# Kernel optimization log

Hardware: AMD Instinct MI355X
Metric: run time of the kernel (lower is better)

The kernel has to match this reference:

```python
import jax, jax.numpy as jnp
import numpy as np

BN_EPS = 1e-5

def conv1x1(w, b, x):
    # w: [O, C], b: [O], x: [B, C, H, W] -> [B, O, H, W]
    return jnp.einsum('oc,bchw->bohw', w, x) + b[None, :, None, None]

def setup_inputs() -> dict:
    key = jax.random.key(0)
    ks = jax.random.split(key, 11)
    C, inter = 256, 128
    B, H, W = 16, 64, 32
    s = 0.05
    return {
        'x': jax.random.normal(ks[0], (B, C, H, W), jnp.float32),
        'g_w': jax.random.normal(ks[1], (inter, C), jnp.float32) * s,
        'g_b': jax.random.normal(ks[2], (inter,), jnp.float32) * s,
        'theta_w': jax.random.normal(ks[3], (inter, C), jnp.float32) * s,
        'theta_b': jax.random.normal(ks[4], (inter,), jnp.float32) * s,
        'phi_w': jax.random.normal(ks[5], (inter, C), jnp.float32) * s,
        'phi_b': jax.random.normal(ks[6], (inter,), jnp.float32) * s,
        'W_w': jax.random.normal(ks[7], (C, inter), jnp.float32) * s,
        'W_b': jax.random.normal(ks[8], (C,), jnp.float32) * s,
        'bn_gamma': jax.random.normal(ks[9], (C,), jnp.float32) * s,
        'bn_beta': jax.random.normal(ks[10], (C,), jnp.float32) * s,
    }

def reference(x, g_w, g_b, theta_w, theta_b, phi_w, phi_b, W_w, W_b, bn_gamma, bn_beta):
    B, C, H, W = x.shape
    N = H * W
    inter = g_w.shape[0]
    # 1x1 conv projections, flattened to token sequences
    g_x = conv1x1(g_w, g_b, x).reshape(B, inter, N).transpose(0, 2, 1)        # [B, N, inter]
    theta_x = conv1x1(theta_w, theta_b, x).reshape(B, inter, N).transpose(0, 2, 1)  # [B, N, inter]
    phi_x = conv1x1(phi_w, phi_b, x).reshape(B, inter, N)                      # [B, inter, N]
    # non-local attention: f = theta @ phi / N, then y = f @ g
    f_div_c = jnp.einsum('bnd,bdm->bnm', theta_x, phi_x) / N                   # [B, N, N]
    y = jnp.einsum('bnm,bmd->bnd', f_div_c, g_x)                               # [B, N, inter]
    y = y.transpose(0, 2, 1).reshape(B, inter, H, W)
    # W: 1x1 conv + BatchNorm (training-mode batch statistics)
    z = conv1x1(W_w, W_b, y)                                                   # [B, C, H, W]
    mean = jnp.mean(z, axis=(0, 2, 3), keepdims=True)
    var = jnp.var(z, axis=(0, 2, 3), keepdims=True)
    z_hat = (z - mean) * jax.lax.rsqrt(var + BN_EPS)
    z_bn = z_hat * bn_gamma[None, :, None, None] + bn_beta[None, :, None, None]
    return z_bn + x
```

## Files before the change

kernel.cpp:

```cpp
#include <hip/hip_runtime.h>

typedef unsigned int uint;
typedef unsigned short ushort;
typedef __attribute__((ext_vector_type(8))) short bf16x8;
typedef __attribute__((ext_vector_type(4))) float f32x4;

#define BB 16
#define CC 256
#define II 128
#define NN 2048
#define BN_EPS 1e-5f

#define OFF_GPART 0
#define OFF_SPART 4194304
#define OFF_CP    4210688
#define OFF_STATP 4214784
#define OFF_STAT2 4345856
#define OFF_PT    4346368
#define OFF_R1    4346624
#define OFF_WGB   4346880
#define OFF_ALPHA 4347136
#define OFF_L1    4347152
#define OFF_R2    4351248
#define OFF_FEND  4355344
#define UGRAM 0
#define UE    1048576
#define UFT   1114112
#define UHT   1179648
#define USBF  2228224
#define UXT   3276800
#define UZ    11665408

static __device__ __forceinline__ ushort f2bf(float f) {
    uint u = __float_as_uint(f);
    return (ushort)((u + 0x7FFFu + ((u >> 16) & 1u)) >> 16);
}
static __device__ __forceinline__ uint pack2(float a, float b) {
    return (uint)f2bf(a) | ((uint)f2bf(b) << 16);
}
static __device__ __forceinline__ float bflo(uint w) { return __uint_as_float(w << 16); }
static __device__ __forceinline__ float bfhi(uint w) { return __uint_as_float(w & 0xFFFF0000u); }
static __device__ __forceinline__ float bfu(ushort u) { return __uint_as_float((uint)u << 16); }

#define MICRO_FMA(av, bv) \
    acc[0][0] += av.x * bv.x; acc[0][1] += av.x * bv.y; acc[0][2] += av.x * bv.z; acc[0][3] += av.x * bv.w; \
    acc[1][0] += av.y * bv.x; acc[1][1] += av.y * bv.y; acc[1][2] += av.y * bv.z; acc[1][3] += av.y * bv.w; \
    acc[2][0] += av.z * bv.x; acc[2][1] += av.z * bv.y; acc[2][2] += av.z * bv.z; acc[2][3] += av.z * bv.w; \
    acc[3][0] += av.w * bv.x; acc[3][1] += av.w * bv.y; acc[3][2] += av.w * bv.z; acc[3][3] += av.w * bv.w;

__global__ __launch_bounds__(256) void convert_xt(
    const float* __restrict__ x, ushort* __restrict__ xT)
{
    __shared__ ushort tile[64][72];
    const int t = threadIdx.x;
    const int b = blockIdx.z, c0 = blockIdx.y * 64, n0 = blockIdx.x * 64;
    const int row = t & 63, ch = t >> 6;
    const size_t srcIdx = ((size_t)(b * CC + c0 + row)) * NN + n0 + ch * 16;
    const float4* sp = (const float4*)(x + srcIdx);
    float4 v0 = sp[0], v1 = sp[1], v2 = sp[2], v3 = sp[3];
    uint p[8];
    p[0] = pack2(v0.x, v0.y); p[1] = pack2(v0.z, v0.w);
    p[2] = pack2(v1.x, v1.y); p[3] = pack2(v1.z, v1.w);
    p[4] = pack2(v2.x, v2.y); p[5] = pack2(v2.z, v2.w);
    p[6] = pack2(v3.x, v3.y); p[7] = pack2(v3.z, v3.w);
    uint* tp = (uint*)&tile[row][ch * 16];
    #pragma unroll
    for (int i = 0; i < 8; ++i) tp[i] = p[i];
    __syncthreads();
    const int trow = t & 63, cch = t >> 6;
    uint q[8];
    #pragma unroll
    for (int i = 0; i < 8; ++i) {
        ushort lo = tile[cch * 16 + 2*i][trow];
        ushort hi = tile[cch * 16 + 2*i + 1][trow];
        q[i] = (uint)lo | ((uint)hi << 16);
    }
    uint4* op = (uint4*)(xT + ((size_t)(b * NN + n0 + trow)) * CC + c0 + cch * 16);
    op[0] = make_uint4(q[0], q[1], q[2], q[3]);
    op[1] = make_uint4(q[4], q[5], q[6], q[7]);
}

__global__ __launch_bounds__(256) void gram_mfma(
    const float* __restrict__ x, float* __restrict__ gpart, float* __restrict__ sPart)
{
    __shared__ ushort As[128][40];
    __shared__ ushort Bs[128][40];
    const int t = threadIdx.x;
    const int jt = blockIdx.x, it = blockIdx.y;
    const int b = blockIdx.z >> 2, kc = blockIdx.z & 3;
    const int iBase = it * 128, jBase = jt * 128;
    const int arow = t >> 1, ah = t & 1;
    const float* aSrc = x + ((size_t)(b * CC + iBase + arow)) * NN + kc * 512 + ah * 16;
    const float* bSrc = x + ((size_t)(b * CC + jBase + arow)) * NN + kc * 512 + ah * 16;
    const int lane = t & 63, wid = t >> 6;
    const int mb = (wid >> 1) * 64, nb = (wid & 1) * 64;
    const int lm = lane & 15, q = lane >> 4;
    f32x4 acc[4][4] = {};
    float ssum = 0.f;

    for (int it16 = 0; it16 < 16; ++it16) {
        const float4* ap = (const float4*)(aSrc + it16 * 32);
        float4 a0 = ap[0], a1 = ap[1], a2 = ap[2], a3 = ap[3];
        const float4* bp = (const float4*)(bSrc + it16 * 32);
        float4 b0 = bp[0], b1 = bp[1], b2 = bp[2], b3 = bp[3];
        uint4 pa0 = { pack2(a0.x,a0.y), pack2(a0.z,a0.w), pack2(a1.x,a1.y), pack2(a1.z,a1.w) };
        uint4 pa1 = { pack2(a2.x,a2.y), pack2(a2.z,a2.w), pack2(a3.x,a3.y), pack2(a3.z,a3.w) };
        uint4 pb0 = { pack2(b0.x,b0.y), pack2(b0.z,b0.w), pack2(b1.x,b1.y), pack2(b1.z,b1.w) };
        uint4 pb1 = { pack2(b2.x,b2.y), pack2(b2.z,b2.w), pack2(b3.x,b3.y), pack2(b3.z,b3.w) };
        *(uint4*)&As[arow][ah * 16]     = pa0;
        *(uint4*)&As[arow][ah * 16 + 8] = pa1;
        *(uint4*)&Bs[arow][ah * 16]     = pb0;
        *(uint4*)&Bs[arow][ah * 16 + 8] = pb1;
        if (jt == 0) {
            ssum += a0.x+a0.y+a0.z+a0.w + a1.x+a1.y+a1.z+a1.w
                  + a2.x+a2.y+a2.z+a2.w + a3.x+a3.y+a3.z+a3.w;
        }
        __syncthreads();
        bf16x8 af[4], bf[4];
        #pragma unroll
        for (int mt = 0; mt < 4; ++mt)
            af[mt] = *(const bf16x8*)&As[mb + mt * 16 + lm][q * 8];
        #pragma unroll
        for (int nt = 0; nt < 4; ++nt)
            bf[nt] = *(const bf16x8*)&Bs[nb + nt * 16 + lm][q * 8];
        #pragma unroll
        for (int mt = 0; mt < 4; ++mt)
            #pragma unroll
            for (int nt = 0; nt < 4; ++nt)
                acc[mt][nt] = __builtin_amdgcn_mfma_f32_16x16x32_bf16(af[mt], bf[nt], acc[mt][nt], 0, 0, 0);
        __syncthreads();
    }
    float* gp = gpart + ((size_t)kc * BB + b) * CC * CC;
    #pragma unroll
    for (int mt = 0; mt < 4; ++mt)
        #pragma unroll
        for (int nt = 0; nt < 4; ++nt)
            #pragma unroll
            for (int r = 0; r < 4; ++r) {
                const int gi = iBase + mb + mt * 16 + q * 4 + r;
                const int gj = jBase + nb + nt * 16 + lm;
                gp[(size_t)gi * CC + gj] = acc[mt][nt][r];
            }
    if (jt == 0) {
        const float so = __shfl_xor(ssum, 1);
        if ((t & 1) == 0)
            sPart[((size_t)kc * BB + b) * CC + iBase + arow] = ssum + so;
    }
}

__global__ __launch_bounds__(256) void gram_reduce(
    const float* __restrict__ gpart, ushort* __restrict__ GramBF)
{
    const int i = blockIdx.x * 256 + threadIdx.x;
    const size_t S = (size_t)BB * CC * CC / 4;
    const float4* p = (const float4*)gpart;
    const float4 a = p[i], b = p[i + S], c = p[i + 2 * S], d = p[i + 3 * S];
    float4 o = { a.x + b.x + c.x + d.x, a.y + b.y + c.y + d.y,
                 a.z + b.z + c.z + d.z, a.w + b.w + c.w + d.w };
    uint2 pk = { pack2(o.x, o.y), pack2(o.z, o.w) };
    ((uint2*)GramBF)[i] = pk;
}

__global__ __launch_bounds__(256) void w1_kernel(
    const float* __restrict__ Ww, const float* __restrict__ Gw,
    const float* __restrict__ Pw, const float* __restrict__ Tw,
    const float* __restrict__ gb, const float* __restrict__ pb, const float* __restrict__ tb,
    ushort* __restrict__ EBF, ushort* __restrict__ FT,
    float* __restrict__ pt, float* __restrict__ r1, float* __restrict__ wgb,
    float* __restrict__ alpha)
{
    const int bz = blockIdx.x;
    const int tid = threadIdx.x;
    if (bz == 32) {
        const int t = tid;
        float ptv = 0.f, r1v = 0.f, wgbv = 0.f;
        for (int d = 0; d < II; ++d) {
            ptv  += Pw[(size_t)d * CC + t] * tb[d];
            r1v  += Tw[(size_t)d * CC + t] * pb[d];
            wgbv += Ww[(size_t)t * II + d] * gb[d];
        }
        pt[t] = ptv; r1[t] = r1v; wgb[t] = wgbv;
        if (t == 0) {
            float al = 0.f;
            for (int d = 0; d < II; ++d) al += pb[d] * tb[d];
            alpha[0] = al;
        }
        return;
    }
    __shared__ float As[32][68];
    __shared__ float Bs[32][68];
    const int a_r = tid >> 2, a_k = (tid & 3) * 8;
    const int b_n = tid & 63, b_k = tid >> 6;
    const int ty = tid >> 4, tx = tid & 15;
    float acc[4][4] = {};
    if (bz < 16) {
        const int cBase = (bz >> 2) * 64, iBase = (bz & 3) * 64;
        const float* ap0 = Ww + (size_t)(cBase + a_r) * II + a_k;
        const float* bp0 = Gw + iBase + b_n;
        for (int k0 = 0; k0 < II; k0 += 32) {
            #pragma unroll
            for (int j = 0; j < 8; ++j) As[a_k + j][a_r] = ap0[k0 + j];
            #pragma unroll
            for (int kk = 0; kk < 8; ++kk) {
                const int k = b_k + kk * 4;
                Bs[k][b_n] = bp0[(size_t)(k0 + k) * CC];
            }
            __syncthreads();
            #pragma unroll
            for (int k = 0; k < 32; ++k) {
                const float4 av = *(const float4*)&As[k][ty * 4];
                const float4 bv = *(const float4*)&Bs[k][tx * 4];
                MICRO_FMA(av, bv)
            }
            __syncthreads();
        }
        #pragma unroll
        for (int ii = 0; ii < 4; ++ii) {
            uint2 o = { pack2(acc[ii][0], acc[ii][1]), pack2(acc[ii][2], acc[ii][3]) };
            *(uint2*)&EBF[(size_t)(cBase + ty * 4 + ii) * CC + iBase + tx * 4] = o;
        }
    } else {
        const int z = bz - 16;
        const int jBase = (z >> 2) * 64, kBase = (z & 3) * 64;
        const float* ap0 = Tw + jBase + b_n;
        const float* bp0 = Pw + kBase + b_n;
        for (int k0 = 0; k0 < II; k0 += 32) {
            #pragma unroll
            for (int kk = 0; kk < 8; ++kk) {
                const int k = b_k + kk * 4;
                As[k][b_n] = ap0[(size_t)(k0 + k) * CC];
                Bs[k][b_n] = bp0[(size_t)(k0 + k) * CC];
            }
            __syncthreads();
            #pragma unroll
            for (int k = 0; k < 32; ++k) {
                const float4 av = *(const float4*)&As[k][ty * 4];
                const float4 bv = *(const float4*)&Bs[k][tx * 4];
                MICRO_FMA(av, bv)
            }
            __syncthreads();
        }
        const float sc = 1.0f / (float)NN;
        #pragma unroll
        for (int ii = 0; ii < 4; ++ii) {
            uint2 o = { pack2(acc[ii][0]*sc, acc[ii][1]*sc), pack2(acc[ii][2]*sc, acc[ii][3]*sc) };
            *(uint2*)&FT[(size_t)(jBase + ty * 4 + ii) * CC + kBase + tx * 4] = o;
        }
    }
}

__global__ __launch_bounds__(256) void u_kernel(
    const float* __restrict__ sPart, const ushort* __restrict__ GramBF,
    const ushort* __restrict__ EBF, const ushort* __restrict__ FT,
    const float* __restrict__ pt, const float* __restrict__ r1,
    const float* __restrict__ wgb, const float* __restrict__ alpha,
    float* __restrict__ cprime, float* __restrict__ L1, float* __restrict__ R2)
{
    __shared__ float sL[256], ptL[256], GptL[256], red[256];
    const int b = blockIdx.x, t = threadIdx.x;
    sL[t] = sPart[(size_t)(0 * BB + b) * CC + t] + sPart[(size_t)(1 * BB + b) * CC + t]
          + sPart[(size_t)(2 * BB + b) * CC + t] + sPart[(size_t)(3 * BB + b) * CC + t];
    ptL[t] = pt[t];
    __syncthreads();
    red[t] = sL[t] * ptL[t];
    __syncthreads();
    for (int s = 128; s > 0; s >>= 1) {
        if (t < s) red[t] += red[t + s];
        __syncthreads();
    }
    const float spt = red[0];
    {
        const uint4* gp = (const uint4*)(GramBF + ((size_t)b * CC + t) * CC);
        float g = 0.f;
        #pragma unroll 4
        for (int kk = 0; kk < 32; ++kk) {
            uint4 v = gp[kk]; const int k = kk * 8;
            g += bflo(v.x)*ptL[k]   + bfhi(v.x)*ptL[k+1] + bflo(v.y)*ptL[k+2] + bfhi(v.y)*ptL[k+3]
               + bflo(v.z)*ptL[k+4] + bfhi(v.z)*ptL[k+5] + bflo(v.w)*ptL[k+6] + bfhi(v.w)*ptL[k+7];
        }
        GptL[t] = g;
    }
    __syncthreads();
    float es = 0.f, eg = 0.f;
    {
        const uint4* ep = (const uint4*)(EBF + (size_t)t * CC);
        #pragma unroll 4
        for (int kk = 0; kk < 32; ++kk) {
            uint4 v = ep[kk]; const int k = kk * 8;
            float e0=bflo(v.x),e1=bfhi(v.x),e2=bflo(v.y),e3=bfhi(v.y);
            float e4=bflo(v.z),e5=bfhi(v.z),e6=bflo(v.w),e7=bfhi(v.w);
            es += e0*sL[k]+e1*sL[k+1]+e2*sL[k+2]+e3*sL[k+3]+e4*sL[k+4]+e5*sL[k+5]+e6*sL[k+6]+e7*sL[k+7];
            eg += e0*GptL[k]+e1*GptL[k+1]+e2*GptL[k+2]+e3*GptL[k+3]+e4*GptL[k+4]+e5*GptL[k+5]+e6*GptL[k+6]+e7*GptL[k+7];
        }
    }
    float r2 = 0.f;
    {
        const uint4* fp = (const uint4*)(FT + (size_t)t * CC);
        #pragma unroll 4
        for (int kk = 0; kk < 32; ++kk) {
            uint4 v = fp[kk]; const int k = kk * 8;
            r2 += bflo(v.x)*sL[k]   + bfhi(v.x)*sL[k+1] + bflo(v.y)*sL[k+2] + bfhi(v.y)*sL[k+3]
                + bflo(v.z)*sL[k+4] + bfhi(v.z)*sL[k+5] + bflo(v.w)*sL[k+6] + bfhi(v.w)*sL[k+7];
        }
    }
    const float al = alpha[0];
    const float wg = wgb[t];
    cprime[b * CC + t] = (eg + al * es + spt * wg) / (float)NN + al * wg;
    L1[b * CC + t] = es / (float)NN;
    R2[b * CC + t] = r2 + r1[t];
}

__global__ __launch_bounds__(256) void h_mfma(
    const ushort* __restrict__ FT, const ushort* __restrict__ GramBF,
    ushort* __restrict__ HT)
{
    __shared__ ushort As[128][40];
    __shared__ ushort Bs[128][40];
    const int t = threadIdx.x;
    const int iBase = blockIdx.x * 128, jBase = blockIdx.y * 128, b = blockIdx.z;
    const int arow = t >> 1, ah = t & 1;
    const ushort* aSrc = FT + (size_t)(jBase + arow) * CC + ah * 16;
    const ushort* bSrc = GramBF + ((size_t)b * CC + iBase + arow) * CC + ah * 16;
    const int lane = t & 63, wid = t >> 6;
    const int mb = (wid >> 1) * 64, nb = (wid & 1) * 64;
    const int lm = lane & 15, q = lane >> 4;
    f32x4 acc[4][4] = {};
    for (int k0 = 0; k0 < CC; k0 += 32) {
        *(uint4*)&As[arow][ah * 16]     = ((const uint4*)(aSrc + k0))[0];
        *(uint4*)&As[arow][ah * 16 + 8] = ((const uint4*)(aSrc + k0))[1];
        *(uint4*)&Bs[arow][ah * 16]     = ((const uint4*)(bSrc + k0))[0];
        *(uint4*)&Bs[arow][ah * 16 + 8] = ((const uint4*)(bSrc + k0))[1];
        __syncthreads();
        bf16x8 af[4], bf[4];
        #pragma unroll
        for (int mt = 0; mt < 4; ++mt)
            af[mt] = *(const bf16x8*)&As[mb + mt * 16 + lm][q * 8];
        #pragma unroll
        for (int nt = 0; nt < 4; ++nt)
            bf[nt] = *(const bf16x8*)&Bs[nb + nt * 16 + lm][q * 8];
        #pragma unroll
        for (int mt = 0; mt < 4; ++mt)
            #pragma unroll
            for (int nt = 0; nt < 4; ++nt)
                acc[mt][nt] = __builtin_amdgcn_mfma_f32_16x16x32_bf16(af[mt], bf[nt], acc[mt][nt], 0, 0, 0);
        __syncthreads();
    }
    ushort* dst = HT + (size_t)b * CC * CC;
    #pragma unroll
    for (int mt = 0; mt < 4; ++mt)
        #pragma unroll
        for (int r = 0; r < 4; ++r) {
            const int j = jBase + mb + mt * 16 + q * 4 + r;
            #pragma unroll
            for (int nt = 0; nt < 4; ++nt) {
                const int i = iBase + nb + nt * 16 + lm;
                dst[(size_t)j * CC + i] = f2bf(acc[mt][nt][r]);
            }
        }
}

__global__ __launch_bounds__(256) void s2_mfma(
    const ushort* __restrict__ EBF, const ushort* __restrict__ HT,
    const float* __restrict__ r1, const float* __restrict__ R2,
    const float* __restrict__ L1, const float* __restrict__ wgb,
    ushort* __restrict__ Sbf)
{
    __shared__ ushort As[128][40];
    __shared__ ushort Bs[128][40];
    const int t = threadIdx.x;
    const int jBase = blockIdx.x * 128, cBase = blockIdx.y * 128, b = blockIdx.z;
    const int arow = t >> 1, ah = t & 1;
    const ushort* aSrc = EBF + (size_t)(cBase + arow) * CC + ah * 16;
    const ushort* bSrc = HT + ((size_t)b * CC + jBase + arow) * CC + ah * 16;
    const int lane = t & 63, wid = t >> 6;
    const int mb = (wid >> 1) * 64, nb = (wid & 1) * 64;
    const int lm = lane & 15, q = lane >> 4;
    f32x4 acc[4][4] = {};
    for (int k0 = 0; k0 < CC; k0 += 32) {
        *(uint4*)&As[arow][ah * 16]     = ((const uint4*)(aSrc + k0))[0];
        *(uint4*)&As[arow][ah * 16 + 8] = ((const uint4*)(aSrc + k0))[1];
        *(uint4*)&Bs[arow][ah * 16]     = ((const uint4*)(bSrc + k0))[0];
        *(uint4*)&Bs[arow][ah * 16 + 8] = ((const uint4*)(bSrc + k0))[1];
        __syncthreads();
        bf16x8 af[4], bf[4];
        #pragma unroll
        for (int mt = 0; mt < 4; ++mt)
            af[mt] = *(const bf16x8*)&As[mb + mt * 16 + lm][q * 8];
        #pragma unroll
        for (int nt = 0; nt < 4; ++nt)
            bf[nt] = *(const bf16x8*)&Bs[nb + nt * 16 + lm][q * 8];
        #pragma unroll
        for (int mt = 0; mt < 4; ++mt)
            #pragma unroll
            for (int nt = 0; nt < 4; ++nt)
                acc[mt][nt] = __builtin_amdgcn_mfma_f32_16x16x32_bf16(af[mt], bf[nt], acc[mt][nt], 0, 0, 0);
        __syncthreads();
    }
    float r1v[4], R2v[4];
    #pragma unroll
    for (int nt = 0; nt < 4; ++nt) {
        const int j = jBase + nb + nt * 16 + lm;
        r1v[nt] = r1[j];
        R2v[nt] = R2[b * CC + j];
    }
    ushort* dst = Sbf + (size_t)b * CC * CC;
    #pragma unroll
    for (int mt = 0; mt < 4; ++mt)
        #pragma unroll
        for (int r = 0; r < 4; ++r) {
            const int c = cBase + mb + mt * 16 + q * 4 + r;
            const float l1v = L1[b * CC + c], wgv = wgb[c];
            #pragma unroll
            for (int nt = 0; nt < 4; ++nt) {
                const int j = jBase + nb + nt * 16 + lm;
                dst[(size_t)c * CC + j] = f2bf(acc[mt][nt][r] + l1v * r1v[nt] + wgv * R2v[nt]);
            }
        }
}

__global__ __launch_bounds__(256) void z_mfma(
    const ushort* __restrict__ Sbf, const ushort* __restrict__ xT,
    const float* __restrict__ cprime, ushort* __restrict__ zbf,
    float* __restrict__ statsPart)
{
    __shared__ ushort As[128][40];
    __shared__ ushort Bs[128][40];
    __shared__ float cpL[128];
    __shared__ float sSum[2][128], sSq[2][128];
    const int t = threadIdx.x;
    const int n0 = blockIdx.x * 128, ct = blockIdx.y * 128, b = blockIdx.z;
    const int arow = t >> 1, ah = t & 1;
    const ushort* aSrc = Sbf + ((size_t)(b * CC + ct + arow)) * CC + ah * 16;
    const ushort* bSrc = xT + ((size_t)(b * NN + n0 + arow)) * CC + ah * 16;
    const int lane = t & 63, wid = t >> 6;
    const int mb = (wid >> 1) * 64, nb = (wid & 1) * 64;
    const int lm = lane & 15, q = lane >> 4;
    f32x4 acc[4][4] = {};

    if (t < 128) cpL[t] = cprime[b * CC + ct + t];

    for (int k0 = 0; k0 < CC; k0 += 32) {
        *(uint4*)&As[arow][ah * 16]     = ((const uint4*)(aSrc + k0))[0];
        *(uint4*)&As[arow][ah * 16 + 8] = ((const uint4*)(aSrc + k0))[1];
        *(uint4*)&Bs[arow][ah * 16]     = ((const uint4*)(bSrc + k0))[0];
        *(uint4*)&Bs[arow][ah * 16 + 8] = ((const uint4*)(bSrc + k0))[1];
        __syncthreads();
        bf16x8 af[4], bf[4];
        #pragma unroll
        for (int mt = 0; mt < 4; ++mt)
            af[mt] = *(const bf16x8*)&As[mb + mt * 16 + lm][q * 8];
        #pragma unroll
        for (int nt = 0; nt < 4; ++nt)
            bf[nt] = *(const bf16x8*)&Bs[nb + nt * 16 + lm][q * 8];
        #pragma unroll
        for (int mt = 0; mt < 4; ++mt)
            #pragma unroll
            for (int nt = 0; nt < 4; ++nt)
                acc[mt][nt] = __builtin_amdgcn_mfma_f32_16x16x32_bf16(af[mt], bf[nt], acc[mt][nt], 0, 0, 0);
        __syncthreads();
    }
    const int nbw = wid & 1;
    #pragma unroll
    for (int mt = 0; mt < 4; ++mt) {
        #pragma unroll
        for (int r = 0; r < 4; ++r) {
            const int cl = mb + mt * 16 + q * 4 + r;
            const int ci = ct + cl;
            const float cp = cpL[cl];
            const size_t zrow = ((size_t)(b * CC + ci)) * NN;
            float s1 = 0.f, q1 = 0.f;
            #pragma unroll
            for (int nt = 0; nt < 4; ++nt) {
                const float val = acc[mt][nt][r] + cp;
                const int tok = n0 + nb + nt * 16 + lm;
                zbf[zrow + tok] = f2bf(val);
                s1 += val; q1 += val * val;
            }
            #pragma unroll
            for (int m = 1; m < 16; m <<= 1) {
                s1 += __shfl_xor(s1, m);
                q1 += __shfl_xor(q1, m);
            }
            if (lm == 0) { sSum[nbw][cl] = s1; sSq[nbw][cl] = q1; }
        }
    }
    __syncthreads();
    if (t < 128) {
        const int slot = blockIdx.z * 16 + blockIdx.x;
        statsPart[(size_t)slot * 512 + ct + t]       = sSum[0][t] + sSum[1][t];
        statsPart[(size_t)slot * 512 + 256 + ct + t] = sSq[0][t] + sSq[1][t];
    }
}

__global__ __launch_bounds__(512) void bn_finalize(
    const float* __restrict__ statsPart, float* __restrict__ stats2)
{
    __shared__ float4 red4[4][128];
    __shared__ float sf[512];
    const int t = threadIdx.x, col = t & 127, grp = t >> 7;
    const float4* sp4 = (const float4*)statsPart;
    float4 a = { 0.f, 0.f, 0.f, 0.f };
    for (int s = grp; s < 256; s += 4) {
        float4 v = sp4[(size_t)s * 128 + col];
        a.x += v.x; a.y += v.y; a.z += v.z; a.w += v.w;
    }
    red4[grp][col] = a;
    __syncthreads();
    if (t < 128) {
        float4 t0 = red4[0][t], t1 = red4[1][t], t2 = red4[2][t], t3 = red4[3][t];
        sf[t*4+0] = t0.x + t1.x + t2.x + t3.x;
        sf[t*4+1] = t0.y + t1.y + t2.y + t3.y;
        sf[t*4+2] = t0.z + t1.z + t2.z + t3.z;
        sf[t*4+3] = t0.w + t1.w + t2.w + t3.w;
    }
    __syncthreads();
    if (t < 256) {
        const float cnt = (float)(BB * NN);
        const float mean = sf[t] / cnt;
        const float var = sf[256 + t] / cnt - mean * mean;
        stats2[t] = mean;
        stats2[CC + t] = rsqrtf(var + BN_EPS);
    }
}

__global__ __launch_bounds__(256) void bn_apply(
    const ushort* __restrict__ zbf, const float* __restrict__ x,
    float* __restrict__ out, const float* __restrict__ stats2,
    const float* __restrict__ gamma, const float* __restrict__ beta)
{
    const size_t i = (size_t)blockIdx.x * 256 + threadIdx.x;
    const size_t base = i * 8;
    const int c = (int)((base >> 11) & (CC - 1));
    const float mean = stats2[c], istd = stats2[CC + c];
    const float gm = gamma[c] * istd;
    const float bt = beta[c] - mean * gm;
    const uint4 zz = *(const uint4*)(zbf + base);
    const float4 x0 = *(const float4*)(x + base);
    const float4 x1 = *(const float4*)(x + base + 4);
    float4 o0, o1;
    o0.x = bflo(zz.x) * gm + bt + x0.x;  o0.y = bfhi(zz.x) * gm + bt + x0.y;
    o0.z = bflo(zz.y) * gm + bt + x0.z;  o0.w = bfhi(zz.y) * gm + bt + x0.w;
    o1.x = bflo(zz.z) * gm + bt + x1.x;  o1.y = bfhi(zz.z) * gm + bt + x1.y;
    o1.z = bflo(zz.w) * gm + bt + x1.z;  o1.w = bfhi(zz.w) * gm + bt + x1.w;
    *(float4*)(out + base) = o0;
    *(float4*)(out + base + 4) = o1;
}

extern "C" void kernel_launch(void* const* d_in, const int* in_sizes, int n_in,
                              void* d_out, int out_size, void* d_ws, size_t ws_size,
                              hipStream_t stream) {
    const float* x    = (const float*)d_in[0];
    const float* g_w  = (const float*)d_in[1];
    const float* g_b  = (const float*)d_in[2];
    const float* th_w = (const float*)d_in[3];
    const float* th_b = (const float*)d_in[4];
    const float* ph_w = (const float*)d_in[5];
    const float* ph_b = (const float*)d_in[6];
    const float* W_w  = (const float*)d_in[7];
    const float* bn_g = (const float*)d_in[9];
    const float* bn_bt= (const float*)d_in[10];
    float* wsf = (float*)d_ws;
    float* out = (float*)d_out;
    ushort* ub = (ushort*)(wsf + OFF_FEND);

    gram_mfma<<<dim3(2, 2, 64), 256, 0, stream>>>(x, wsf + OFF_GPART, wsf + OFF_SPART);
    convert_xt<<<dim3(32, 4, 16), 256, 0, stream>>>(x, ub + UXT);
    gram_reduce<<<dim3(1024), 256, 0, stream>>>(wsf + OFF_GPART, ub + UGRAM);
    w1_kernel<<<dim3(33), 256, 0, stream>>>(W_w, g_w, ph_w, th_w, g_b, ph_b, th_b,
        ub + UE, ub + UFT, wsf + OFF_PT, wsf + OFF_R1, wsf + OFF_WGB, wsf + OFF_ALPHA);
    u_kernel<<<dim3(16), 256, 0, stream>>>(wsf + OFF_SPART, ub + UGRAM, ub + UE, ub + UFT,
        wsf + OFF_PT, wsf + OFF_R1, wsf + OFF_WGB, wsf + OFF_ALPHA,
        wsf + OFF_CP, wsf + OFF_L1, wsf + OFF_R2);
    h_mfma<<<dim3(2, 2, 16), 256, 0, stream>>>(ub + UFT, ub + UGRAM, ub + UHT);
    s2_mfma<<<dim3(2, 2, 16), 256, 0, stream>>>(ub + UE, ub + UHT,
        wsf + OFF_R1, wsf + OFF_R2, wsf + OFF_L1, wsf + OFF_WGB, ub + USBF);
    z_mfma<<<dim3(16, 2, 16), 256, 0, stream>>>(ub + USBF, ub + UXT,
        wsf + OFF_CP, ub + UZ, wsf + OFF_STATP);
    bn_finalize<<<dim3(1), 512, 0, stream>>>(wsf + OFF_STATP, wsf + OFF_STAT2);
    bn_apply<<<dim3(4096), 256, 0, stream>>>(ub + UZ, x, out, wsf + OFF_STAT2, bn_g, bn_bt);
}
```

Before: 225.3 us.

## Merge gram, transpose, weight prep and reductions into fewer fused kernels

Folds the gram GEMM, the x transpose/convert, and the weight-preprocessing kernel into one launch, and splits the gram K dimension 8 ways for more blocks. On diagonal tiles the second operand load is skipped and the transpose is emitted from shared memory. The gram reduction merges with the u kernel, which now reads the fp32 partials directly. h and s2 fuse into one kernel that keeps the intermediate in LDS, and BN finalize is spread over 4 blocks. Fewer launches and less intermediate traffic come at the cost of doubled partial-gram memory and a large LDS footprint in the fused S kernel.

```diff
diff --git a/kernel.cpp b/kernel.cpp
--- a/kernel.cpp
+++ b/kernel.cpp
@@ -12,24 +12,23 @@
 #define BN_EPS 1e-5f
 
 #define OFF_GPART 0
-#define OFF_SPART 4194304
-#define OFF_CP    4210688
-#define OFF_STATP 4214784
-#define OFF_STAT2 4345856
-#define OFF_PT    4346368
-#define OFF_R1    4346624
-#define OFF_WGB   4346880
-#define OFF_ALPHA 4347136
-#define OFF_L1    4347152
-#define OFF_R2    4351248
-#define OFF_FEND  4355344
+#define OFF_SPART 8388608
+#define OFF_CP    8421376
+#define OFF_STATP 8425472
+#define OFF_STAT2 8556544
+#define OFF_PT    8557056
+#define OFF_R1    8557312
+#define OFF_WGB   8557568
+#define OFF_ALPHA 8557824
+#define OFF_L1    8558080
+#define OFF_R2    8562176
+#define OFF_FEND  8566272
 #define UGRAM 0
 #define UE    1048576
 #define UFT   1114112
-#define UHT   1179648
-#define USBF  2228224
-#define UXT   3276800
-#define UZ    11665408
+#define USBF  1179648
+#define UXT   2228224
+#define UZ    10616832
 
 static __device__ __forceinline__ ushort f2bf(float f) {
     uint u = __float_as_uint(f);
@@ -40,7 +39,6 @@
 }
 static __device__ __forceinline__ float bflo(uint w) { return __uint_as_float(w << 16); }
 static __device__ __forceinline__ float bfhi(uint w) { return __uint_as_float(w & 0xFFFF0000u); }
-static __device__ __forceinline__ float bfu(ushort u) { return __uint_as_float((uint)u << 16); }
 
 #define MICRO_FMA(av, bv) \
     acc[0][0] += av.x * bv.x; acc[0][1] += av.x * bv.y; acc[0][2] += av.x * bv.z; acc[0][3] += av.x * bv.w; \
@@ -48,131 +46,107 @@
     acc[2][0] += av.z * bv.x; acc[2][1] += av.z * bv.y; acc[2][2] += av.z * bv.z; acc[2][3] += av.z * bv.w; \
     acc[3][0] += av.w * bv.x; acc[3][1] += av.w * bv.y; acc[3][2] += av.w * bv.z; acc[3][3] += av.w * bv.w;
 
-__global__ __launch_bounds__(256) void convert_xt(
-    const float* __restrict__ x, ushort* __restrict__ xT)
-{
-    __shared__ ushort tile[64][72];
-    const int t = threadIdx.x;
-    const int b = blockIdx.z, c0 = blockIdx.y * 64, n0 = blockIdx.x * 64;
-    const int row = t & 63, ch = t >> 6;
-    const size_t srcIdx = ((size_t)(b * CC + c0 + row)) * NN + n0 + ch * 16;
-    const float4* sp = (const float4*)(x + srcIdx);
-    float4 v0 = sp[0], v1 = sp[1], v2 = sp[2], v3 = sp[3];
-    uint p[8];
-    p[0] = pack2(v0.x, v0.y); p[1] = pack2(v0.z, v0.w);
-    p[2] = pack2(v1.x, v1.y); p[3] = pack2(v1.z, v1.w);
-    p[4] = pack2(v2.x, v2.y); p[5] = pack2(v2.z, v2.w);
-    p[6] = pack2(v3.x, v3.y); p[7] = pack2(v3.z, v3.w);
-    uint* tp = (uint*)&tile[row][ch * 16];
-    #pragma unroll
-    for (int i = 0; i < 8; ++i) tp[i] = p[i];
-    __syncthreads();
-    const int trow = t & 63, cch = t >> 6;
-    uint q[8];
-    #pragma unroll
-    for (int i = 0; i < 8; ++i) {
-        ushort lo = tile[cch * 16 + 2*i][trow];
-        ushort hi = tile[cch * 16 + 2*i + 1][trow];
-        q[i] = (uint)lo | ((uint)hi << 16);
-    }
-    uint4* op = (uint4*)(xT + ((size_t)(b * NN + n0 + trow)) * CC + c0 + cch * 16);
-    op[0] = make_uint4(q[0], q[1], q[2], q[3]);
-    op[1] = make_uint4(q[4], q[5], q[6], q[7]);
-}
-
-__global__ __launch_bounds__(256) void gram_mfma(
-    const float* __restrict__ x, float* __restrict__ gpart, float* __restrict__ sPart)
-{
-    __shared__ ushort As[128][40];
-    __shared__ ushort Bs[128][40];
-    const int t = threadIdx.x;
-    const int jt = blockIdx.x, it = blockIdx.y;
-    const int b = blockIdx.z >> 2, kc = blockIdx.z & 3;
-    const int iBase = it * 128, jBase = jt * 128;
-    const int arow = t >> 1, ah = t & 1;
-    const float* aSrc = x + ((size_t)(b * CC + iBase + arow)) * NN + kc * 512 + ah * 16;
-    const float* bSrc = x + ((size_t)(b * CC + jBase + arow)) * NN + kc * 512 + ah * 16;
-    const int lane = t & 63, wid = t >> 6;
-    const int mb = (wid >> 1) * 64, nb = (wid & 1) * 64;
-    const int lm = lane & 15, q = lane >> 4;
-    f32x4 acc[4][4] = {};
-    float ssum = 0.f;
-
-    for (int it16 = 0; it16 < 16; ++it16) {
-        const float4* ap = (const float4*)(aSrc + it16 * 32);
-        float4 a0 = ap[0], a1 = ap[1], a2 = ap[2], a3 = ap[3];
-        const float4* bp = (const float4*)(bSrc + it16 * 32);
-        float4 b0 = bp[0], b1 = bp[1], b2 = bp[2], b3 = bp[3];
-        uint4 pa0 = { pack2(a0.x,a0.y), pack2(a0.z,a0.w), pack2(a1.x,a1.y), pack2(a1.z,a1.w) };
-        uint4 pa1 = { pack2(a2.x,a2.y), pack2(a2.z,a2.w), pack2(a3.x,a3.y), pack2(a3.z,a3.w) };
-        uint4 pb0 = { pack2(b0.x,b0.y), pack2(b0.z,b0.w), pack2(b1.x,b1.y), pack2(b1.z,b1.w) };
-        uint4 pb1 = { pack2(b2.x,b2.y), pack2(b2.z,b2.w), pack2(b3.x,b3.y), pack2(b3.z,b3.w) };
-        *(uint4*)&As[arow][ah * 16]     = pa0;
-        *(uint4*)&As[arow][ah * 16 + 8] = pa1;
-        *(uint4*)&Bs[arow][ah * 16]     = pb0;
-        *(uint4*)&Bs[arow][ah * 16 + 8] = pb1;
-        if (jt == 0) {
-            ssum += a0.x+a0.y+a0.z+a0.w + a1.x+a1.y+a1.z+a1.w
-                  + a2.x+a2.y+a2.z+a2.w + a3.x+a3.y+a3.z+a3.w;
-        }
-        __syncthreads();
-        bf16x8 af[4], bf[4];
-        #pragma unroll
-        for (int mt = 0; mt < 4; ++mt)
-            af[mt] = *(const bf16x8*)&As[mb + mt * 16 + lm][q * 8];
-        #pragma unroll
-        for (int nt = 0; nt < 4; ++nt)
-            bf[nt] = *(const bf16x8*)&Bs[nb + nt * 16 + lm][q * 8];
-        #pragma unroll
-        for (int mt = 0; mt < 4; ++mt)
-            #pragma unroll
-            for (int nt = 0; nt < 4; ++nt)
-                acc[mt][nt] = __builtin_amdgcn_mfma_f32_16x16x32_bf16(af[mt], bf[nt], acc[mt][nt], 0, 0, 0);
-        __syncthreads();
-    }
-    float* gp = gpart + ((size_t)kc * BB + b) * CC * CC;
-    #pragma unroll
-    for (int mt = 0; mt < 4; ++mt)
-        #pragma unroll
-        for (int nt = 0; nt < 4; ++nt)
-            #pragma unroll
-            for (int r = 0; r < 4; ++r) {
-                const int gi = iBase + mb + mt * 16 + q * 4 + r;
-                const int gj = jBase + nb + nt * 16 + lm;
-                gp[(size_t)gi * CC + gj] = acc[mt][nt][r];
-            }
-    if (jt == 0) {
-        const float so = __shfl_xor(ssum, 1);
-        if ((t & 1) == 0)
-            sPart[((size_t)kc * BB + b) * CC + iBase + arow] = ssum + so;
-    }
-}
-
-__global__ __launch_bounds__(256) void gram_reduce(
-    const float* __restrict__ gpart, ushort* __restrict__ GramBF)
-{
-    const int i = blockIdx.x * 256 + threadIdx.x;
-    const size_t S = (size_t)BB * CC * CC / 4;
-    const float4* p = (const float4*)gpart;
-    const float4 a = p[i], b = p[i + S], c = p[i + 2 * S], d = p[i + 3 * S];
-    float4 o = { a.x + b.x + c.x + d.x, a.y + b.y + c.y + d.y,
-                 a.z + b.z + c.z + d.z, a.w + b.w + c.w + d.w };
-    uint2 pk = { pack2(o.x, o.y), pack2(o.z, o.w) };
-    ((uint2*)GramBF)[i] = pk;
-}
-
-__global__ __launch_bounds__(256) void w1_kernel(
+__global__ __launch_bounds__(256) void mega1(
+    const float* __restrict__ x,
     const float* __restrict__ Ww, const float* __restrict__ Gw,
     const float* __restrict__ Pw, const float* __restrict__ Tw,
     const float* __restrict__ gb, const float* __restrict__ pb, const float* __restrict__ tb,
+    float* __restrict__ gpart, float* __restrict__ sPart, ushort* __restrict__ xT,
     ushort* __restrict__ EBF, ushort* __restrict__ FT,
     float* __restrict__ pt, float* __restrict__ r1, float* __restrict__ wgb,
     float* __restrict__ alpha)
 {
-    const int bz = blockIdx.x;
-    const int tid = threadIdx.x;
+    __shared__ __align__(16) char smem[20480];
+    const int bid = blockIdx.x;
+    const int t = threadIdx.x;
+
+    if (bid < 512) {
+        ushort (*As)[40] = (ushort(*)[40])smem;
+        ushort (*Bs)[40] = (ushort(*)[40])(smem + 10240);
+        const int jt = bid & 1, it = (bid >> 1) & 1;
+        const int z = bid >> 2;
+        const int b = z >> 3, kc = z & 7;
+        const int iBase = it * 128, jBase = jt * 128;
+        const bool diag = (it == jt);
+        const int arow = t >> 1, ah = t & 1;
+        const float* aSrc = x + ((size_t)(b * CC + iBase + arow)) * NN + kc * 256 + ah * 16;
+        const float* bSrc = x + ((size_t)(b * CC + jBase + arow)) * NN + kc * 256 + ah * 16;
+        const int lane = t & 63, wid = t >> 6;
+        const int mb = (wid >> 1) * 64, nb = (wid & 1) * 64;
+        const int lm = lane & 15, q = lane >> 4;
+        f32x4 acc[4][4] = {};
+        float ssum = 0.f;
+
+        for (int it16 = 0; it16 < 8; ++it16) {
+            const float4* ap = (const float4*)(aSrc + it16 * 32);
+            float4 a0 = ap[0], a1 = ap[1], a2 = ap[2], a3 = ap[3];
+            uint4 pa0 = { pack2(a0.x,a0.y), pack2(a0.z,a0.w), pack2(a1.x,a1.y), pack2(a1.z,a1.w) };
+            uint4 pa1 = { pack2(a2.x,a2.y), pack2(a2.z,a2.w), pack2(a3.x,a3.y), pack2(a3.z,a3.w) };
+            *(uint4*)&As[arow][ah * 16]     = pa0;
+            *(uint4*)&As[arow][ah * 16 + 8] = pa1;
+            if (!diag) {
+                const float4* bp = (const float4*)(bSrc + it16 * 32);
+                float4 b0 = bp[0], b1 = bp[1], b2 = bp[2], b3 = bp[3];
+                uint4 pb0 = { pack2(b0.x,b0.y), pack2(b0.z,b0.w), pack2(b1.x,b1.y), pack2(b1.z,b1.w) };
+                uint4 pb1 = { pack2(b2.x,b2.y), pack2(b2.z,b2.w), pack2(b3.x,b3.y), pack2(b3.z,b3.w) };
+                *(uint4*)&Bs[arow][ah * 16]     = pb0;
+                *(uint4*)&Bs[arow][ah * 16 + 8] = pb1;
+            }
+            if (jt == 0) {
+                ssum += a0.x+a0.y+a0.z+a0.w + a1.x+a1.y+a1.z+a1.w
+                      + a2.x+a2.y+a2.z+a2.w + a3.x+a3.y+a3.z+a3.w;
+            }
+            __syncthreads();
+            const ushort (*Bsel)[40] = diag ? (const ushort(*)[40])As : (const ushort(*)[40])Bs;
+            bf16x8 af[4], bf[4];
+            #pragma unroll
+            for (int mt = 0; mt < 4; ++mt)
+                af[mt] = *(const bf16x8*)&As[mb + mt * 16 + lm][q * 8];
+            #pragma unroll
+            for (int nt = 0; nt < 4; ++nt)
+                bf[nt] = *(const bf16x8*)&Bsel[nb + nt * 16 + lm][q * 8];
+            #pragma unroll
+            for (int mt = 0; mt < 4; ++mt)
+                #pragma unroll
+                for (int nt = 0; nt < 4; ++nt)
+                    acc[mt][nt] = __builtin_amdgcn_mfma_f32_16x16x32_bf16(af[mt], bf[nt], acc[mt][nt], 0, 0, 0);
+            if (diag) {
+                const int n_l = t & 31, cg = t >> 5;
+                uint qv[8];
+                #pragma unroll
+                for (int i2 = 0; i2 < 8; ++i2) {
+                    ushort lo = As[cg * 16 + 2*i2][n_l];
+                    ushort hi = As[cg * 16 + 2*i2 + 1][n_l];
+                    qv[i2] = (uint)lo | ((uint)hi << 16);
+                }
+                const int ng = kc * 256 + it16 * 32 + n_l;
+                uint4* op = (uint4*)(xT + ((size_t)(b * NN + ng)) * CC + iBase + cg * 16);
+                op[0] = make_uint4(qv[0], qv[1], qv[2], qv[3]);
+                op[1] = make_uint4(qv[4], qv[5], qv[6], qv[7]);
+            }
+            __syncthreads();
+        }
+        float* gp = gpart + ((size_t)kc * BB + b) * CC * CC;
+        #pragma unroll
+        for (int mt = 0; mt < 4; ++mt)
+            #pragma unroll
+            for (int nt = 0; nt < 4; ++nt)
+                #pragma unroll
+                for (int r = 0; r < 4; ++r) {
+                    const int gi = iBase + mb + mt * 16 + q * 4 + r;
+                    const int gj = jBase + nb + nt * 16 + lm;
+                    gp[(size_t)gi * CC + gj] = acc[mt][nt][r];
+                }
+        if (jt == 0) {
+            const float so = __shfl_xor(ssum, 1);
+            if ((t & 1) == 0)
+                sPart[((size_t)kc * BB + b) * CC + iBase + arow] = ssum + so;
+        }
+        return;
+    }
+
+    const int bz = bid - 512;
     if (bz == 32) {
-        const int t = tid;
         float ptv = 0.f, r1v = 0.f, wgbv = 0.f;
         for (int d = 0; d < II; ++d) {
             ptv  += Pw[(size_t)d * CC + t] * tb[d];
@@ -187,11 +161,11 @@
         }
         return;
     }
-    __shared__ float As[32][68];
-    __shared__ float Bs[32][68];
-    const int a_r = tid >> 2, a_k = (tid & 3) * 8;
-    const int b_n = tid & 63, b_k = tid >> 6;
-    const int ty = tid >> 4, tx = tid & 15;
+    float (*As)[68] = (float(*)[68])smem;
+    float (*Bs)[68] = (float(*)[68])(smem + 8704);
+    const int a_r = t >> 2, a_k = (t & 3) * 8;
+    const int b_n = t & 63, b_k = t >> 6;
+    const int ty = t >> 4, tx = t & 15;
     float acc[4][4] = {};
     if (bz < 16) {
         const int cBase = (bz >> 2) * 64, iBase = (bz & 3) * 64;
@@ -220,8 +194,8 @@
             *(uint2*)&EBF[(size_t)(cBase + ty * 4 + ii) * CC + iBase + tx * 4] = o;
         }
     } else {
-        const int z = bz - 16;
-        const int jBase = (z >> 2) * 64, kBase = (z & 3) * 64;
+        const int zz = bz - 16;
+        const int jBase = (zz >> 2) * 64, kBase = (zz & 3) * 64;
         const float* ap0 = Tw + jBase + b_n;
         const float* bp0 = Pw + kBase + b_n;
         for (int k0 = 0; k0 < II; k0 += 32) {
@@ -249,18 +223,39 @@
     }
 }
 
-__global__ __launch_bounds__(256) void u_kernel(
-    const float* __restrict__ sPart, const ushort* __restrict__ GramBF,
+__global__ __launch_bounds__(256) void mega2(
+    const float* __restrict__ gpart, const float* __restrict__ sPart,
     const ushort* __restrict__ EBF, const ushort* __restrict__ FT,
     const float* __restrict__ pt, const float* __restrict__ r1,
     const float* __restrict__ wgb, const float* __restrict__ alpha,
+    ushort* __restrict__ GramBF,
     float* __restrict__ cprime, float* __restrict__ L1, float* __restrict__ R2)
 {
-    __shared__ float sL[256], ptL[256], GptL[256], red[256];
-    const int b = blockIdx.x, t = threadIdx.x;
-    sL[t] = sPart[(size_t)(0 * BB + b) * CC + t] + sPart[(size_t)(1 * BB + b) * CC + t]
-          + sPart[(size_t)(2 * BB + b) * CC + t] + sPart[(size_t)(3 * BB + b) * CC + t];
-    ptL[t] = pt[t];
+    const int bid = blockIdx.x;
+    const int t = threadIdx.x;
+    if (bid < 1024) {
+        const int i = bid * 256 + t;
+        const size_t S = (size_t)BB * CC * CC / 4;
+        const float4* p = (const float4*)gpart;
+        float4 o = { 0.f, 0.f, 0.f, 0.f };
+        #pragma unroll
+        for (int k = 0; k < 8; ++k) {
+            float4 v = p[i + (size_t)k * S];
+            o.x += v.x; o.y += v.y; o.z += v.z; o.w += v.w;
+        }
+        uint2 pk = { pack2(o.x, o.y), pack2(o.z, o.w) };
+        ((uint2*)GramBF)[i] = pk;
+        return;
+    }
+    const int b = bid - 1024;
+    __shared__ __align__(16) float sL[256], ptL[256], GptL[256], red[256];
+    {
+        float s = 0.f;
+        #pragma unroll
+        for (int kc = 0; kc < 8; ++kc) s += sPart[((size_t)kc * BB + b) * CC + t];
+        sL[t] = s;
+        ptL[t] = pt[t];
+    }
     __syncthreads();
     red[t] = sL[t] * ptL[t];
     __syncthreads();
@@ -269,16 +264,20 @@
         __syncthreads();
     }
     const float spt = red[0];
+    const int lane = t & 63, wv = t >> 6;
     {
-        const uint4* gp = (const uint4*)(GramBF + ((size_t)b * CC + t) * CC);
-        float g = 0.f;
-        #pragma unroll 4
-        for (int kk = 0; kk < 32; ++kk) {
-            uint4 v = gp[kk]; const int k = kk * 8;
-            g += bflo(v.x)*ptL[k]   + bfhi(v.x)*ptL[k+1] + bflo(v.y)*ptL[k+2] + bfhi(v.y)*ptL[k+3]
-               + bflo(v.z)*ptL[k+4] + bfhi(v.z)*ptL[k+5] + bflo(v.w)*ptL[k+6] + bfhi(v.w)*ptL[k+7];
-        }
-        GptL[t] = g;
+        const float4 pt4 = *(const float4*)&ptL[lane * 4];
+        for (int r = wv; r < 256; r += 4) {
+            float a = 0.f;
+            #pragma unroll
+            for (int kc = 0; kc < 8; ++kc) {
+                const float4 g = *(const float4*)&gpart[(((size_t)kc * BB + b) * CC + r) * CC + lane * 4];
+                a += g.x * pt4.x + g.y * pt4.y + g.z * pt4.z + g.w * pt4.w;
+            }
+            #pragma unroll
+            for (int m = 32; m > 0; m >>= 1) a += __shfl_xor(a, m);
+            if (lane == 0) GptL[r] = a;
+        }
     }
     __syncthreads();
     float es = 0.f, eg = 0.f;
@@ -310,82 +309,69 @@
     R2[b * CC + t] = r2 + r1[t];
 }
 
-__global__ __launch_bounds__(256) void h_mfma(
-    const ushort* __restrict__ FT, const ushort* __restrict__ GramBF,
-    ushort* __restrict__ HT)
-{
-    __shared__ ushort As[128][40];
-    __shared__ ushort Bs[128][40];
-    const int t = threadIdx.x;
-    const int iBase = blockIdx.x * 128, jBase = blockIdx.y * 128, b = blockIdx.z;
-    const int arow = t >> 1, ah = t & 1;
-    const ushort* aSrc = FT + (size_t)(jBase + arow) * CC + ah * 16;
-    const ushort* bSrc = GramBF + ((size_t)b * CC + iBase + arow) * CC + ah * 16;
-    const int lane = t & 63, wid = t >> 6;
-    const int mb = (wid >> 1) * 64, nb = (wid & 1) * 64;
-    const int lm = lane & 15, q = lane >> 4;
-    f32x4 acc[4][4] = {};
-    for (int k0 = 0; k0 < CC; k0 += 32) {
-        *(uint4*)&As[arow][ah * 16]     = ((const uint4*)(aSrc + k0))[0];
-        *(uint4*)&As[arow][ah * 16 + 8] = ((const uint4*)(aSrc + k0))[1];
-        *(uint4*)&Bs[arow][ah * 16]     = ((const uint4*)(bSrc + k0))[0];
-        *(uint4*)&Bs[arow][ah * 16 + 8] = ((const uint4*)(bSrc + k0))[1];
-        __syncthreads();
-        bf16x8 af[4], bf[4];
-        #pragma unroll
-        for (int mt = 0; mt < 4; ++mt)
-            af[mt] = *(const bf16x8*)&As[mb + mt * 16 + lm][q * 8];
-        #pragma unroll
-        for (int nt = 0; nt < 4; ++nt)
-            bf[nt] = *(const bf16x8*)&Bs[nb + nt * 16 + lm][q * 8];
-        #pragma unroll
-        for (int mt = 0; mt < 4; ++mt)
-            #pragma unroll
-            for (int nt = 0; nt < 4; ++nt)
-                acc[mt][nt] = __builtin_amdgcn_mfma_f32_16x16x32_bf16(af[mt], bf[nt], acc[mt][nt], 0, 0, 0);
-        __syncthreads();
-    }
-    ushort* dst = HT + (size_t)b * CC * CC;
-    #pragma unroll
-    for (int mt = 0; mt < 4; ++mt)
-        #pragma unroll
-        for (int r = 0; r < 4; ++r) {
-            const int j = jBase + mb + mt * 16 + q * 4 + r;
-            #pragma unroll
-            for (int nt = 0; nt < 4; ++nt) {
-                const int i = iBase + nb + nt * 16 + lm;
-                dst[(size_t)j * CC + i] = f2bf(acc[mt][nt][r]);
-            }
-        }
-}
-
-__global__ __launch_bounds__(256) void s2_mfma(
-    const ushort* __restrict__ EBF, const ushort* __restrict__ HT,
+__global__ __launch_bounds__(256) void sfused(
+    const ushort* __restrict__ EBF, const ushort* __restrict__ GramBF,
+    const ushort* __restrict__ FT,
     const float* __restrict__ r1, const float* __restrict__ R2,
     const float* __restrict__ L1, const float* __restrict__ wgb,
     ushort* __restrict__ Sbf)
 {
     __shared__ ushort As[128][40];
     __shared__ ushort Bs[128][40];
+    __shared__ ushort Qs[128][264];
     const int t = threadIdx.x;
-    const int jBase = blockIdx.x * 128, cBase = blockIdx.y * 128, b = blockIdx.z;
+    const int b = blockIdx.x >> 2;
+    const int ct = (blockIdx.x >> 1) & 1, jt = blockIdx.x & 1;
+    const int cBase = ct * 128, jBase = jt * 128;
     const int arow = t >> 1, ah = t & 1;
-    const ushort* aSrc = EBF + (size_t)(cBase + arow) * CC + ah * 16;
-    const ushort* bSrc = HT + ((size_t)b * CC + jBase + arow) * CC + ah * 16;
     const int lane = t & 63, wid = t >> 6;
     const int mb = (wid >> 1) * 64, nb = (wid & 1) * 64;
     const int lm = lane & 15, q = lane >> 4;
+    const ushort* aSrc = EBF + (size_t)(cBase + arow) * CC + ah * 16;
+
+    #pragma unroll
+    for (int half = 0; half < 2; ++half) {
+        const ushort* bSrc = GramBF + ((size_t)b * CC + half * 128 + arow) * CC + ah * 16;
+        f32x4 acc[4][4] = {};
+        for (int k0 = 0; k0 < CC; k0 += 32) {
+            *(uint4*)&As[arow][ah * 16]     = ((const uint4*)(aSrc + k0))[0];
+            *(uint4*)&As[arow][ah * 16 + 8] = ((const uint4*)(aSrc + k0))[1];
+            *(uint4*)&Bs[arow][ah * 16]     = ((const uint4*)(bSrc + k0))[0];
+            *(uint4*)&Bs[arow][ah * 16 + 8] = ((const uint4*)(bSrc + k0))[1];
+            __syncthreads();
+            bf16x8 af[4], bf[4];
+            #pragma unroll
+            for (int mt = 0; mt < 4; ++mt)
+                af[mt] = *(const bf16x8*)&As[mb + mt * 16 + lm][q * 8];
+            #pragma unroll
+            for (int nt = 0; nt < 4; ++nt)
+                bf[nt] = *(const bf16x8*)&Bs[nb + nt * 16 + lm][q * 8];
+            #pragma unroll
+            for (int mt = 0; mt < 4; ++mt)
+                #pragma unroll
+                for (int nt = 0; nt < 4; ++nt)
+                    acc[mt][nt] = __builtin_amdgcn_mfma_f32_16x16x32_bf16(af[mt], bf[nt], acc[mt][nt], 0, 0, 0);
+            __syncthreads();
+        }
+        #pragma unroll
+        for (int mt = 0; mt < 4; ++mt)
+            #pragma unroll
+            for (int nt = 0; nt < 4; ++nt)
+                #pragma unroll
+                for (int r = 0; r < 4; ++r)
+                    Qs[mb + mt * 16 + q * 4 + r][half * 128 + nb + nt * 16 + lm] = f2bf(acc[mt][nt][r]);
+        __syncthreads();
+    }
     f32x4 acc[4][4] = {};
+    const ushort* fSrc = FT + (size_t)(jBase + arow) * CC + ah * 16;
     for (int k0 = 0; k0 < CC; k0 += 32) {
-        *(uint4*)&As[arow][ah * 16]     = ((const uint4*)(aSrc + k0))[0];
-        *(uint4*)&As[arow][ah * 16 + 8] = ((const uint4*)(aSrc + k0))[1];
-        *(uint4*)&Bs[arow][ah * 16]     = ((const uint4*)(bSrc + k0))[0];
-        *(uint4*)&Bs[arow][ah * 16 + 8] = ((const uint4*)(bSrc + k0))[1];
+        *(uint4*)&Bs[arow][ah * 16]     = ((const uint4*)(fSrc + k0))[0];
+        *(uint4*)&Bs[arow][ah * 16 + 8] = ((const uint4*)(fSrc + k0))[1];
         __syncthreads();
         bf16x8 af[4], bf[4];
         #pragma unroll
         for (int mt = 0; mt < 4; ++mt)
-            af[mt] = *(const bf16x8*)&As[mb + mt * 16 + lm][q * 8];
+            af[mt] = *(const bf16x8*)&Qs[mb + mt * 16 + lm][k0 + q * 8];
         #pragma unroll
         for (int nt = 0; nt < 4; ++nt)
             bf[nt] = *(const bf16x8*)&Bs[nb + nt * 16 + lm][q * 8];
@@ -495,31 +481,26 @@
 __global__ __launch_bounds__(512) void bn_finalize(
     const float* __restrict__ statsPart, float* __restrict__ stats2)
 {
-    __shared__ float4 red4[4][128];
-    __shared__ float sf[512];
-    const int t = threadIdx.x, col = t & 127, grp = t >> 7;
-    const float4* sp4 = (const float4*)statsPart;
-    float4 a = { 0.f, 0.f, 0.f, 0.f };
-    for (int s = grp; s < 256; s += 4) {
-        float4 v = sp4[(size_t)s * 128 + col];
-        a.x += v.x; a.y += v.y; a.z += v.z; a.w += v.w;
-    }
-    red4[grp][col] = a;
+    __shared__ float red[4][128];
+    __shared__ float sf[128];
+    const int g = blockIdx.x;
+    const int t = threadIdx.x;
+    const int cl = t & 127, sg = t >> 7;
+    const int col = (cl < 64) ? (g * 64 + cl) : (256 + g * 64 + (cl - 64));
+    float a = 0.f;
+    for (int s = sg * 64; s < sg * 64 + 64; ++s)
+        a += statsPart[(size_t)s * 512 + col];
+    red[sg][cl] = a;
     __syncthreads();
-    if (t < 128) {
-        float4 t0 = red4[0][t], t1 = red4[1][t], t2 = red4[2][t], t3 = red4[3][t];
-        sf[t*4+0] = t0.x + t1.x + t2.x + t3.x;
-        sf[t*4+1] = t0.y + t1.y + t2.y + t3.y;
-        sf[t*4+2] = t0.z + t1.z + t2.z + t3.z;
-        sf[t*4+3] = t0.w + t1.w + t2.w + t3.w;
-    }
+    if (t < 128) sf[t] = red[0][t] + red[1][t] + red[2][t] + red[3][t];
     __syncthreads();
-    if (t < 256) {
+    if (t < 64) {
         const float cnt = (float)(BB * NN);
         const float mean = sf[t] / cnt;
-        const float var = sf[256 + t] / cnt - mean * mean;
-        stats2[t] = mean;
-        stats2[CC + t] = rsqrtf(var + BN_EPS);
+        const float var = sf[64 + t] / cnt - mean * mean;
+        const int c = g * 64 + t;
+        stats2[c] = mean;
+        stats2[CC + c] = rsqrtf(var + BN_EPS);
     }
 }
 
@@ -563,19 +544,20 @@
     float* out = (float*)d_out;
     ushort* ub = (ushort*)(wsf + OFF_FEND);
 
-    gram_mfma<<<dim3(2, 2, 64), 256, 0, stream>>>(x, wsf + OFF_GPART, wsf + OFF_SPART);
-    convert_xt<<<dim3(32, 4, 16), 256, 0, stream>>>(x, ub + UXT);
-    gram_reduce<<<dim3(1024), 256, 0, stream>>>(wsf + OFF_GPART, ub + UGRAM);
-    w1_kernel<<<dim3(33), 256, 0, stream>>>(W_w, g_w, ph_w, th_w, g_b, ph_b, th_b,
-        ub + UE, ub + UFT, wsf + OFF_PT, wsf + OFF_R1, wsf + OFF_WGB, wsf + OFF_ALPHA);
-    u_kernel<<<dim3(16), 256, 0, stream>>>(wsf + OFF_SPART, ub + UGRAM, ub + UE, ub + UFT,
+    mega1<<<dim3(545), 256, 0, stream>>>(
+        x, W_w, g_w, ph_w, th_w, g_b, ph_b, th_b,
+        wsf + OFF_GPART, wsf + OFF_SPART, ub + UXT,
+        ub + UE, ub + UFT,
+        wsf + OFF_PT, wsf + OFF_R1, wsf + OFF_WGB, wsf + OFF_ALPHA);
+    mega2<<<dim3(1040), 256, 0, stream>>>(
+        wsf + OFF_GPART, wsf + OFF_SPART, ub + UE, ub + UFT,
         wsf + OFF_PT, wsf + OFF_R1, wsf + OFF_WGB, wsf + OFF_ALPHA,
-        wsf + OFF_CP, wsf + OFF_L1, wsf + OFF_R2);
-    h_mfma<<<dim3(2, 2, 16), 256, 0, stream>>>(ub + UFT, ub + UGRAM, ub + UHT);
-    s2_mfma<<<dim3(2, 2, 16), 256, 0, stream>>>(ub + UE, ub + UHT,
+        ub + UGRAM, wsf + OFF_CP, wsf + OFF_L1, wsf + OFF_R2);
+    sfused<<<dim3(64), 256, 0, stream>>>(
+        ub + UE, ub + UGRAM, ub + UFT,
         wsf + OFF_R1, wsf + OFF_R2, wsf + OFF_L1, wsf + OFF_WGB, ub + USBF);
-    z_mfma<<<dim3(16, 2, 16), 256, 0, stream>>>(ub + USBF, ub + UXT,
-        wsf + OFF_CP, ub + UZ, wsf + OFF_STATP);
-    bn_finalize<<<dim3(1), 512, 0, stream>>>(wsf + OFF_STATP, wsf + OFF_STAT2);
+    z_mfma<<<dim3(16, 2, 16), 256, 0, stream>>>(
+        ub + USBF, ub + UXT, wsf + OFF_CP, ub + UZ, wsf + OFF_STATP);
+    bn_finalize<<<dim3(4), 512, 0, stream>>>(wsf + OFF_STATP, wsf + OFF_STAT2);
     bn_apply<<<dim3(4096), 256, 0, stream>>>(ub + UZ, x, out, wsf + OFF_STAT2, bn_g, bn_bt);
 }
```

Measured after the change: 231.1 us. +2.6%, slower.
